# Kernel tuning notes

Measured on AMD Instinct MI355X. Metric: run time of the kernel, lower is better.

The kernel has to match this reference:

```python
import jax, jax.numpy as jnp
import numpy as np

B, S, H = 1, 2048, 2048
NH = 16
NOPE, ROPE, VD = 128, 64, 128
QD = NOPE + ROPE
QLR, KVLR = 1536, 512
INH, IND, ITOPK = 4, 32, 512
EPS = 1e-6
SCALE = QD ** -0.5
ISCALE = IND ** -0.5


def rms_norm(x, w, eps=EPS):
    x = x * jax.lax.rsqrt(jnp.mean(x * x, axis=-1, keepdims=True) + eps)
    return w * x


def rotate_half(x):
    h = x.shape[-1] // 2
    return jnp.concatenate([-x[..., h:], x[..., :h]], axis=-1)


def setup_inputs():
    key = jax.random.key(0)
    ks = jax.random.split(key, 9)
    # real RoPE tables, theta=10000
    inv = 1.0 / (10000.0 ** (np.arange(0, ROPE, 2, dtype=np.float64) / ROPE))
    freqs = np.outer(np.arange(S, dtype=np.float64), inv)
    emb = np.concatenate([freqs, freqs], axis=-1)
    return {
        "x": jax.random.normal(ks[0], (B, S, H), jnp.float32),
        "cos": jnp.asarray(np.cos(emb), jnp.float32),
        "sin": jnp.asarray(np.sin(emb), jnp.float32),
        "q_a_w": jax.random.normal(ks[1], (QLR, H), jnp.float32) * 0.02,
        "q_a_norm_w": jnp.ones((QLR,), jnp.float32),
        "q_b_w": jax.random.normal(ks[2], (NH * QD, QLR), jnp.float32) * 0.02,
        "kv_a_w": jax.random.normal(ks[3], (KVLR + ROPE, H), jnp.float32) * 0.02,
        "kv_a_norm_w": jnp.ones((KVLR,), jnp.float32),
        "kv_b_w": jax.random.normal(ks[4], (NH * (NOPE + VD), KVLR), jnp.float32) * 0.02,
        "o_w": jax.random.normal(ks[5], (H, NH * VD), jnp.float32) * 0.02,
        "idx_q_w": jax.random.normal(ks[6], (INH * IND, H), jnp.float32) * 0.02,
        "idx_k_w": jax.random.normal(ks[7], (INH * IND, H), jnp.float32) * 0.02,
    }


def mla_forward(x, cos, sin, q_a_w, q_a_norm_w, q_b_w, kv_a_w, kv_a_norm_w,
                kv_b_w, o_w, idx_q_w, idx_k_w):
    b, s, _ = x.shape
    # low-rank Q: q_b(norm(q_a(x)))
    q = rms_norm(x @ q_a_w.T, q_a_norm_w) @ q_b_w.T
    q = q.reshape(b, s, NH, QD).transpose(0, 2, 1, 3)          # [b,H,s,QD]
    q_nope, q_pe = q[..., :NOPE], q[..., NOPE:]
    # low-rank KV: kv_a -> (compressed_kv, k_pe)
    kv_a = x @ kv_a_w.T                                         # [b,s,KVLR+ROPE]
    compressed_kv, k_pe = kv_a[..., :KVLR], kv_a[..., KVLR:]
    k_pe = k_pe[:, None]                                        # [b,1,s,ROPE]
    kv = (rms_norm(compressed_kv, kv_a_norm_w) @ kv_b_w.T)
    kv = kv.reshape(b, s, NH, NOPE + VD).transpose(0, 2, 1, 3)  # [b,H,s,NOPE+VD]
    k_nope, v = kv[..., :NOPE], kv[..., NOPE:]
    # decoupled RoPE on the rope sub-dim only
    c, sn = cos[None, None], sin[None, None]                    # [1,1,s,ROPE]
    q_pe = q_pe * c + rotate_half(q_pe) * sn
    k_pe = k_pe * c + rotate_half(k_pe) * sn
    qf = jnp.concatenate([q_nope, q_pe], axis=-1)               # [b,H,s,QD]
    kf = jnp.concatenate(
        [k_nope, jnp.broadcast_to(k_pe, (b, NH, s, ROPE))], axis=-1)
    scores = jnp.einsum('bhqd,bhkd->bhqk', qf, kf) * SCALE
    # indexer: mean-over-heads scores -> top-k allowed key positions per query
    iq = (x @ idx_q_w.T).reshape(b, s, INH, IND).transpose(0, 2, 1, 3)
    ik = (x @ idx_k_w.T).reshape(b, s, INH, IND).transpose(0, 2, 1, 3)
    iscores = jnp.einsum('bhqd,bhkd->bhqk', iq, ik) * ISCALE
    iscores = iscores.mean(axis=1)                              # [b,s,s]
    _, topk_idx = jax.lax.top_k(iscores, ITOPK)                 # [b,s,topk]
    allowed = jnp.zeros((b, s, s), bool).at[
        jnp.arange(b)[:, None, None],
        jnp.arange(s)[None, :, None],
        topk_idx].set(True)
    causal = jnp.tril(jnp.ones((s, s), bool))
    mask = allowed[:, None] & causal[None, None]                # [b,1,s,s] & causal
    scores = jnp.where(mask, scores, jnp.float32(-1e9))
    attn = jax.nn.softmax(scores, axis=-1)
    out = jnp.einsum('bhqk,bhkd->bhqd', attn, v)
    out = out.transpose(0, 2, 1, 3).reshape(b, s, NH * VD)
    return out @ o_w.T


def reference(x, cos, sin, q_a_w, q_a_norm_w, q_b_w, kv_a_w, kv_a_norm_w,
              kv_b_w, o_w, idx_q_w, idx_k_w):
    return mla_forward(x, cos, sin, q_a_w, q_a_norm_w, q_b_w, kv_a_w,
                       kv_a_norm_w, kv_b_w, o_w, idx_q_w, idx_k_w)
```

## Files before the change

### kernel.cpp

```cpp
#include <hip/hip_runtime.h>
#include <hip/hip_bf16.h>
#include <stdint.h>

#define S_LEN  2048
#define NHEADS 16
#define D_NOPE 128
#define D_ROPE 64
#define D_V    128
#define D_Q    192
#define ITOPK  512

static constexpr float ATT_SCALE = 0.07216878364870322f;
static constexpr float ISC4      = 0.04419417382415922f;
static constexpr float RMS_EPS   = 1e-6f;

typedef __bf16 bf16x8 __attribute__((ext_vector_type(8)));
typedef float  f32x4  __attribute__((ext_vector_type(4)));

__device__ __forceinline__ float b2f(unsigned short u) {
    union { unsigned int i; float f; } x; x.i = ((unsigned int)u) << 16; return x.f;
}
__device__ __forceinline__ unsigned short f2b(float f) {
    union { float f; unsigned int i; } x; x.f = f;
    unsigned int lsb = (x.i >> 16) & 1;
    x.i += 0x7fffu + lsb;
    return (unsigned short)(x.i >> 16);
}

__device__ __forceinline__ void gload16(const unsigned short* g, unsigned short* l)
{
    __builtin_amdgcn_global_load_lds(
        (const __attribute__((address_space(1))) unsigned int*)g,
        (__attribute__((address_space(3))) unsigned int*)l, 16, 0, 0);
}

__global__ __launch_bounds__(256)
void cast_f32_bf16(const float* __restrict__ src, unsigned short* __restrict__ dst, int n4)
{
    int i = blockIdx.x * 256 + threadIdx.x;
    if (i < n4) {
        float4 v = ((const float4*)src)[i];
        ushort4 o;
        o.x = f2b(v.x); o.y = f2b(v.y); o.z = f2b(v.z); o.w = f2b(v.w);
        ((ushort4*)dst)[i] = o;
    }
}

__global__ __launch_bounds__(256)
void gemm_f32_nt(const float* __restrict__ A, int lda,
                 const float* __restrict__ B, int ldb,
                 float* __restrict__ C, int M, int N, float alpha, int kChunk)
{
    __shared__ float As[16][132];
    __shared__ float Bs[16][132];
    const int row0 = blockIdx.y * 128;
    const int col0 = blockIdx.x * 128;
    const int t  = threadIdx.x;
    const int tx = t & 15, ty = t >> 4;
    const int kStart = blockIdx.z * kChunk;
    C += (size_t)blockIdx.z * M * N;

    float acc[8][8] = {};

    for (int k0 = kStart; k0 < kStart + kChunk; k0 += 16) {
#pragma unroll
        for (int i = 0; i < 2; i++) {
            int f = t + i * 256;
            int r = f >> 2;
            int kq = (f & 3) << 2;
            int gr = row0 + r;
            float4 va = make_float4(0.f, 0.f, 0.f, 0.f);
            if (gr < M) va = *(const float4*)(A + (size_t)gr * lda + k0 + kq);
            As[kq + 0][r] = va.x; As[kq + 1][r] = va.y;
            As[kq + 2][r] = va.z; As[kq + 3][r] = va.w;
            int gc = col0 + r;
            float4 vb = make_float4(0.f, 0.f, 0.f, 0.f);
            if (gc < N) vb = *(const float4*)(B + (size_t)gc * ldb + k0 + kq);
            Bs[kq + 0][r] = vb.x; Bs[kq + 1][r] = vb.y;
            Bs[kq + 2][r] = vb.z; Bs[kq + 3][r] = vb.w;
        }
        __syncthreads();
#pragma unroll
        for (int kk = 0; kk < 16; kk++) {
            float4 A0 = *(const float4*)&As[kk][ty * 8];
            float4 A1 = *(const float4*)&As[kk][ty * 8 + 4];
            float4 B0 = *(const float4*)&Bs[kk][tx * 8];
            float4 B1 = *(const float4*)&Bs[kk][tx * 8 + 4];
            float a[8] = {A0.x, A0.y, A0.z, A0.w, A1.x, A1.y, A1.z, A1.w};
            float b[8] = {B0.x, B0.y, B0.z, B0.w, B1.x, B1.y, B1.z, B1.w};
#pragma unroll
            for (int i = 0; i < 8; i++)
#pragma unroll
                for (int j = 0; j < 8; j++)
                    acc[i][j] = fmaf(a[i], b[j], acc[i][j]);
        }
        __syncthreads();
    }

#pragma unroll
    for (int i = 0; i < 8; i++) {
        int r = row0 + ty * 8 + i;
        if (r >= M) continue;
#pragma unroll
        for (int j = 0; j < 8; j++) {
            int c = col0 + tx * 8 + j;
            if (c >= N) continue;
            C[(size_t)r * N + c] = acc[i][j] * alpha;
        }
    }
}

__global__ __launch_bounds__(256)
void reduceN_k(const float* __restrict__ p, float* __restrict__ out, int n4, int parts)
{
    int i = blockIdx.x * 256 + threadIdx.x;
    if (i < n4) {
        const float4* a = (const float4*)p;
        float4 o = a[i];
        for (int z = 1; z < parts; z++) {
            float4 r = a[i + (size_t)z * n4];
            o.x += r.x; o.y += r.y; o.z += r.z; o.w += r.w;
        }
        ((float4*)out)[i] = o;
    }
}

template<bool OUTBF16>
__global__ __launch_bounds__(256)
void gemm_bf16_nt(const unsigned short* __restrict__ A, int lda, int aStep,
                  const unsigned short* __restrict__ B, int ldb, int bStep,
                  void* __restrict__ Cv, int ldc, int cStep,
                  int M, int N, int K, float alpha)
{
    __shared__ unsigned short As[128 * 32];
    __shared__ unsigned short Bs[128 * 32];
    A += (size_t)blockIdx.z * aStep;
    B += (size_t)blockIdx.z * bStep;
    unsigned short* Cb = (unsigned short*)Cv + (size_t)blockIdx.z * cStep;
    float*          Cf = (float*)Cv          + (size_t)blockIdx.z * cStep;

    const int t = threadIdx.x;
    const int row0 = blockIdx.y * 128, col0 = blockIdx.x * 128;
    const int w = t >> 6, l = t & 63;
    const int wr = (w >> 1) * 64, wc = (w & 1) * 64;
    const int fr = l & 15, fk = l >> 4;

    f32x4 acc[4][4] = {};

    const int sr = t >> 2, ss = t & 3;

    for (int k0 = 0; k0 < K; k0 += 32) {
#pragma unroll
        for (int c = 0; c < 2; c++) {
            int r  = sr + c * 64;
            int ga = min(row0 + r, M - 1);
            int gb = min(col0 + r, N - 1);
            gload16(A + (size_t)ga * lda + k0 + ss * 8, As + (c * 256 + t) * 8);
            gload16(B + (size_t)gb * ldb + k0 + ss * 8, Bs + (c * 256 + t) * 8);
        }
        __syncthreads();

        bf16x8 af[4], bfr[4];
#pragma unroll
        for (int mi = 0; mi < 4; mi++) {
            int ra = wr + mi * 16 + fr;
            af[mi] = *(const bf16x8*)((const char*)As + ra * 64 + fk * 16);
        }
#pragma unroll
        for (int nj = 0; nj < 4; nj++) {
            int rb = wc + nj * 16 + fr;
            bfr[nj] = *(const bf16x8*)((const char*)Bs + rb * 64 + fk * 16);
        }
#pragma unroll
        for (int mi = 0; mi < 4; mi++)
#pragma unroll
            for (int nj = 0; nj < 4; nj++)
                acc[mi][nj] = __builtin_amdgcn_mfma_f32_16x16x32_bf16(
                                  af[mi], bfr[nj], acc[mi][nj], 0, 0, 0);
        __syncthreads();
    }

#pragma unroll
    for (int mi = 0; mi < 4; mi++)
#pragma unroll
        for (int nj = 0; nj < 4; nj++)
#pragma unroll
            for (int rg = 0; rg < 4; rg++) {
                int rr = row0 + wr + mi * 16 + fk * 4 + rg;
                int cc = col0 + wc + nj * 16 + fr;
                if (rr < M && cc < N) {
                    float v = acc[mi][nj][rg] * alpha;
                    if constexpr (OUTBF16) Cb[(size_t)rr * ldc + cc] = f2b(v);
                    else                   Cf[(size_t)rr * ldc + cc] = v;
                }
            }
}

__global__ __launch_bounds__(256)
void rms_bf16_inplace(unsigned short* x, const float* __restrict__ w, int n)
{
    __shared__ float red[256];
    const int row = blockIdx.x, t = threadIdx.x;
    unsigned short* ip = x + (size_t)row * n;
    float ss = 0.f;
    for (int i = t; i < n; i += 256) { float v = b2f(ip[i]); ss = fmaf(v, v, ss); }
    red[t] = ss; __syncthreads();
    for (int s2 = 128; s2; s2 >>= 1) { if (t < s2) red[t] += red[t + s2]; __syncthreads(); }
    float rs = rsqrtf(red[0] / (float)n + RMS_EPS);
    for (int i = t; i < n; i += 256) ip[i] = f2b(b2f(ip[i]) * rs * w[i]);
}

__global__ __launch_bounds__(256)
void rms_f32_bf16(const float* __restrict__ in, unsigned short* __restrict__ out,
                  const float* __restrict__ w, int n, int in_stride, int out_stride)
{
    __shared__ float red[256];
    const int row = blockIdx.x, t = threadIdx.x;
    const float* ip = in + (size_t)row * in_stride;
    float ss = 0.f;
    for (int i = t; i < n; i += 256) { float v = ip[i]; ss = fmaf(v, v, ss); }
    red[t] = ss; __syncthreads();
    for (int s2 = 128; s2; s2 >>= 1) { if (t < s2) red[t] += red[t + s2]; __syncthreads(); }
    float rs = rsqrtf(red[0] / (float)n + RMS_EPS);
    unsigned short* op = out + (size_t)row * out_stride;
    for (int i = t; i < n; i += 256) op[i] = f2b(ip[i] * rs * w[i]);
}

__global__ __launch_bounds__(256)
void rope_q_k(const unsigned short* __restrict__ qbuf, const float* __restrict__ cosb,
              const float* __restrict__ sinb, unsigned short* __restrict__ qec)
{
    int idx = blockIdx.x * 256 + threadIdx.x;
    int s = idx >> 9, h = (idx >> 5) & 15, d = idx & 31;
    const unsigned short* qp = qbuf + ((size_t)s * NHEADS + h) * D_Q + D_NOPE;
    float x1 = b2f(qp[d]), x2 = b2f(qp[d + 32]);
    const float* cr = cosb + (size_t)s * D_ROPE;
    const float* sr = sinb + (size_t)s * D_ROPE;
    unsigned short* op = qec + ((size_t)s * NHEADS + h) * 576 + 512;
    op[d]      = f2b(x1 * cr[d]      - x2 * sr[d]);
    op[d + 32] = f2b(x2 * cr[d + 32] + x1 * sr[d + 32]);
}

__global__ __launch_bounds__(256)
void rope_kpe_k(const float* __restrict__ kv_a, const float* __restrict__ cosb,
                const float* __restrict__ sinb, unsigned short* __restrict__ klat)
{
    int idx = blockIdx.x * 256 + threadIdx.x;
    int s = idx >> 5, d = idx & 31;
    const float* kp = kv_a + (size_t)s * 576 + 512;
    float x1 = kp[d], x2 = kp[d + 32];
    const float* cr = cosb + (size_t)s * D_ROPE;
    const float* sr = sinb + (size_t)s * D_ROPE;
    unsigned short* op = klat + (size_t)s * 576 + 512;
    op[d]      = f2b(x1 * cr[d]      - x2 * sr[d]);
    op[d + 32] = f2b(x2 * cr[d + 32] + x1 * sr[d + 32]);
}

__global__ __launch_bounds__(256)
void wkt_k(const unsigned short* __restrict__ kvbw, unsigned short* __restrict__ wkt)
{
    __shared__ unsigned short tile[32][520];
    const int h = blockIdx.x, dc = blockIdx.y, t = threadIdx.x;
    for (int i = t; i < 32 * 64; i += 256) {
        int d = i >> 6, c8 = (i & 63) * 8;
        uint4 v = *(const uint4*)(kvbw + ((size_t)(h * 256 + dc * 32 + d)) * 512 + c8);
        *(uint4*)&tile[d][c8] = v;
    }
    __syncthreads();
    for (int i = t; i < 512 * 4; i += 256) {
        int c = i >> 2, d8 = (i & 3) * 8;
        unsigned short tmp[8];
#pragma unroll
        for (int j = 0; j < 8; j++) tmp[j] = tile[d8 + j][c];
        *(uint4*)(wkt + ((size_t)h * 512 + c) * 128 + dc * 32 + d8) = *(uint4*)tmp;
    }
}

__global__ __launch_bounds__(256)
void ckvsum_k(const unsigned short* __restrict__ klat, float* __restrict__ part)
{
    const int b = blockIdx.x, t = threadIdx.x;
    float s0 = 0.f, s1 = 0.f;
    for (int r = 0; r < 128; r++) {
        const unsigned short* row = klat + (size_t)(b * 128 + r) * 576;
        s0 += b2f(row[t]); s1 += b2f(row[t + 256]);
    }
    part[b * 512 + t] = s0; part[b * 512 + t + 256] = s1;
}
__global__ __launch_bounds__(256)
void ckvmean_k(const float* __restrict__ part, float* __restrict__ mean)
{
    int t = blockIdx.x * 256 + threadIdx.x;
    if (t < 512) {
        float s = 0.f;
        for (int b = 0; b < 16; b++) s += part[b * 512 + t];
        mean[t] = s * (1.f / 2048.f);
    }
}

__global__ __launch_bounds__(256)
void topk_mask_k(const float* __restrict__ iscores, uint32_t* __restrict__ mask)
{
    const int q = blockIdx.x, t = threadIdx.x;
    const int w = t >> 6, l = t & 63;
    __shared__ uint32_t u[S_LEN];
    __shared__ int hist4[4][256];
    __shared__ int sfx[257];
    __shared__ int wtot[4];
    __shared__ uint32_t mw[64];
    __shared__ int sh_b, sh_R;

    for (int i = t; i < S_LEN; i += 256) {
        uint32_t b = __float_as_uint(iscores[(size_t)q * S_LEN + i]);
        u[i] = (b & 0x80000000u) ? ~b : (b | 0x80000000u);
    }
    if (t < 64) mw[t] = 0u;

    uint32_t prefix = 0;
    int R = ITOPK;
#pragma unroll 1
    for (int shift = 24; shift >= 0; shift -= 8) {
        hist4[0][t] = 0; hist4[1][t] = 0; hist4[2][t] = 0; hist4[3][t] = 0;
        __syncthreads();
        uint32_t pmask = (shift == 24) ? 0u : (0xFFFFFFFFu << (shift + 8));
        for (int i = t; i < S_LEN; i += 256) {
            uint32_t v = u[i];
            if ((v & pmask) == prefix)
                atomicAdd(&hist4[w][(v >> shift) & 255], 1);
        }
        __syncthreads();
        int x = hist4[0][255 - t] + hist4[1][255 - t] + hist4[2][255 - t] + hist4[3][255 - t];
#pragma unroll
        for (int d = 1; d < 64; d <<= 1) {
            int y = __shfl_up(x, d);
            if (l >= d) x += y;
        }
        if (l == 63) wtot[w] = x;
        __syncthreads();
        for (int ww = 0; ww < w; ww++) x += wtot[ww];
        sfx[255 - t] = x;
        if (t == 0) sfx[256] = 0;
        __syncthreads();
        if (sfx[t] >= R && sfx[t + 1] < R) { sh_b = t; sh_R = R - sfx[t + 1]; }
        __syncthreads();
        prefix |= (uint32_t)sh_b << shift;
        R = sh_R;
        __syncthreads();
    }
    const uint32_t T = prefix;
    const int need = R;

    for (int i = t; i < S_LEN; i += 256) {
        uint32_t v = u[i];
        bool sel = v > T;
        if (!sel && v == T) {
            int rank = 0;
            for (int j = 0; j < i; j++) rank += (u[j] == T) ? 1 : 0;
            sel = rank < need;
        }
        if (sel) atomicOr(&mw[i >> 5], 1u << (i & 31));
    }
    __syncthreads();
    if (t < 64) mask[(size_t)q * 64 + t] = mw[t];
}

__global__ __launch_bounds__(256, 4)
void attn_lat_k(const unsigned short* __restrict__ qec,
                const unsigned short* __restrict__ klat,
                const uint32_t* __restrict__ mask,
                const float* __restrict__ ckvmean,
                unsigned short* __restrict__ ov)
{
    const int qi = blockIdx.x, t = threadIdx.x;
    const int w = t >> 6, l = t & 63;
    const int c16 = l & 15, g = l >> 4;

    __shared__ unsigned short kl[512];
    __shared__ uint32_t wds[64];
    __shared__ int pfx[65];
    __shared__ float wred[4][16];
    __shared__ float linv[16];
    __shared__ unsigned short PB[16][520];
    __shared__ unsigned short CT[256][40];

    kl[t] = 0; kl[t + 256] = 0;
    if (t < 64) {
        uint32_t wd = mask[(size_t)qi * 64 + t];
        int rem = qi - t * 32;
        if (rem < 0) wd = 0u;
        else if (rem < 31) wd &= ((2u << rem) - 1u);
        wds[t] = wd;
        pfx[t] = __popc(wd);
    }
    __syncthreads();
    if (t == 0) {
        int s = 0;
        for (int i = 0; i < 64; i++) { int cc = pfx[i]; pfx[i] = s; s += cc; }
        pfx[64] = s;
    }
    __syncthreads();
    const int nv = pfx[64];

    if (nv == 0) {
        for (int i = t; i < 16 * 512; i += 256) {
            int h = i >> 9, c = i & 511;
            ov[((size_t)qi * 16 + h) * 512 + c] = f2b(ckvmean[c]);
        }
        return;
    }

    if (t < 64) {
        int pos = pfx[t];
        uint32_t wd = wds[t];
        while (wd) { int b = __ffs(wd) - 1; wd &= wd - 1; kl[pos++] = (unsigned short)(t * 32 + b); }
    }
    __syncthreads();

    const int ntile = (nv + 63) >> 6;

    f32x4 acc[8] = {};
    uint32_t kb[8];
#pragma unroll
    for (int tt = 0; tt < 8; tt++)
        kb[tt] = (uint32_t)kl[tt * 64 + w * 16 + c16] * 1152u;

    const unsigned short* qrow = qec + (size_t)qi * (16 * 576);
#pragma unroll 2
    for (int ks = 0; ks < 18; ks++) {
        bf16x8 af = *(const bf16x8*)(qrow + c16 * 576 + ks * 32 + g * 8);
#pragma unroll
        for (int tt = 0; tt < 8; tt++) {
            if (tt < ntile) {
                bf16x8 bf = *(const bf16x8*)((const char*)klat + (kb[tt] + (uint32_t)(ks * 64 + g * 16)));
                acc[tt] = __builtin_amdgcn_mfma_f32_16x16x32_bf16(af, bf, acc[tt], 0, 0, 0);
            }
        }
    }

    float m4[4];
#pragma unroll
    for (int r = 0; r < 4; r++) {
        float mm = -1e30f;
#pragma unroll
        for (int tt = 0; tt < 8; tt++) {
            if (tt < ntile) {
                int kp = tt * 64 + w * 16 + c16;
                float s = (kp < nv) ? acc[tt][r] * ATT_SCALE : -1e30f;
                acc[tt][r] = s;
                mm = fmaxf(mm, s);
            }
        }
#pragma unroll
        for (int o = 8; o; o >>= 1) mm = fmaxf(mm, __shfl_xor(mm, o));
        m4[r] = mm;
    }
    if (c16 == 0) {
#pragma unroll
        for (int r = 0; r < 4; r++) wred[w][g * 4 + r] = m4[r];
    }
    __syncthreads();
#pragma unroll
    for (int r = 0; r < 4; r++) {
        int h = g * 4 + r;
        m4[r] = fmaxf(fmaxf(wred[0][h], wred[1][h]), fmaxf(wred[2][h], wred[3][h]));
    }
    __syncthreads();

    float s4[4] = {0.f, 0.f, 0.f, 0.f};
#pragma unroll
    for (int tt = 0; tt < 8; tt++) {
        if (tt < ntile) {
            int kp = tt * 64 + w * 16 + c16;
#pragma unroll
            for (int r = 0; r < 4; r++) {
                float e = __expf(acc[tt][r] - m4[r]);
                s4[r] += e;
                PB[g * 4 + r][kp] = f2b(e);
            }
        }
    }
#pragma unroll
    for (int r = 0; r < 4; r++) {
        float ss = s4[r];
#pragma unroll
        for (int o = 8; o; o >>= 1) ss += __shfl_xor(ss, o);
        s4[r] = ss;
    }
    if (c16 == 0) {
#pragma unroll
        for (int r = 0; r < 4; r++) wred[w][g * 4 + r] = s4[r];
    }
    __syncthreads();
    if (t < 16) linv[t] = 1.f / (wred[0][t] + wred[1][t] + wred[2][t] + wred[3][t]);

    f32x4 pv[8] = {};
    const int nkc = (nv + 31) >> 5;
    const int k2 = t >> 4, lg = t & 15;
    const int cp = (k2 ^ ((lg & 3) << 2)) * 2;
    uint4 stg[4];

#define LOADKEYS(HT, KC) do { \
        uint32_t kb0 = (uint32_t)kl[(KC) * 32 + 2 * k2] * 1152u; \
        uint32_t kb1 = (uint32_t)kl[(KC) * 32 + 2 * k2 + 1] * 1152u; \
        const uint4* s0 = (const uint4*)((const char*)klat + kb0 + (HT) * 512 + lg * 32); \
        const uint4* s1 = (const uint4*)((const char*)klat + kb1 + (HT) * 512 + lg * 32); \
        stg[0] = s0[0]; stg[1] = s0[1]; stg[2] = s1[0]; stg[3] = s1[1]; \
    } while (0)

    LOADKEYS(0, 0);
#pragma unroll
    for (int ht = 0; ht < 2; ht++) {
        for (int kc = 0; kc < nkc; kc++) {
            __syncthreads();
            {
#pragma unroll
                for (int v4 = 0; v4 < 2; v4++) {
                    uint4 a4 = stg[v4], b4 = stg[v4 + 2];
                    int la = lg * 16 + v4 * 8;
                    *(uint32_t*)&CT[la + 0][cp] = (a4.x & 0xFFFFu) | (b4.x << 16);
                    *(uint32_t*)&CT[la + 1][cp] = (a4.x >> 16) | (b4.x & 0xFFFF0000u);
                    *(uint32_t*)&CT[la + 2][cp] = (a4.y & 0xFFFFu) | (b4.y << 16);
                    *(uint32_t*)&CT[la + 3][cp] = (a4.y >> 16) | (b4.y & 0xFFFF0000u);
                    *(uint32_t*)&CT[la + 4][cp] = (a4.z & 0xFFFFu) | (b4.z << 16);
                    *(uint32_t*)&CT[la + 5][cp] = (a4.z >> 16) | (b4.z & 0xFFFF0000u);
                    *(uint32_t*)&CT[la + 6][cp] = (a4.w & 0xFFFFu) | (b4.w << 16);
                    *(uint32_t*)&CT[la + 7][cp] = (a4.w >> 16) | (b4.w & 0xFFFF0000u);
                }
            }
            if (kc + 1 < nkc) LOADKEYS(ht, kc + 1);
            else if (ht == 0) LOADKEYS(1, 0);
            __syncthreads();
            bf16x8 pa = *(const bf16x8*)(&PB[c16][kc * 32 + g * 8]);
            __builtin_amdgcn_s_setprio(1);
#pragma unroll
            for (int nt = 0; nt < 4; nt++) {
                int rowh = w * 64 + nt * 16 + c16;
                bf16x8 cb = *(const bf16x8*)(&CT[rowh][(g ^ nt) * 8]);
                pv[ht * 4 + nt] = __builtin_amdgcn_mfma_f32_16x16x32_bf16(
                                      pa, cb, pv[ht * 4 + nt], 0, 0, 0);
            }
            __builtin_amdgcn_s_setprio(0);
        }
    }
#undef LOADKEYS

#pragma unroll
    for (int ht = 0; ht < 2; ht++)
#pragma unroll
        for (int nt = 0; nt < 4; nt++)
#pragma unroll
            for (int r = 0; r < 4; r++) {
                int h = g * 4 + r;
                int lat = ht * 256 + w * 64 + nt * 16 + c16;
                ov[((size_t)qi * 16 + h) * 512 + lat] = f2b(pv[ht * 4 + nt][r] * linv[h]);
            }
}

extern "C" void kernel_launch(void* const* d_in, const int* in_sizes, int n_in,
                              void* d_out, int out_size, void* d_ws, size_t ws_size,
                              hipStream_t stream)
{
    const float* x       = (const float*)d_in[0];
    const float* cosb    = (const float*)d_in[1];
    const float* sinb    = (const float*)d_in[2];
    const float* q_a_w   = (const float*)d_in[3];
    const float* q_a_nw  = (const float*)d_in[4];
    const float* q_b_w   = (const float*)d_in[5];
    const float* kv_a_w  = (const float*)d_in[6];
    const float* kv_a_nw = (const float*)d_in[7];
    const float* kv_b_w  = (const float*)d_in[8];
    const float* o_w     = (const float*)d_in[9];
    const float* idx_q_w = (const float*)d_in[10];
    const float* idx_k_w = (const float*)d_in[11];
    (void)in_sizes; (void)n_in; (void)out_size; (void)ws_size;

    typedef unsigned short u16;
    char* ws = (char*)d_ws;
    u16*      xb   = (u16*)(ws + 0);
    u16*      qaw  = (u16*)(ws + 8388608);
    u16*      kvaw = (u16*)(ws + 14680064);
    u16*      qbw  = (u16*)(ws + 17039360);
    u16*      q_a  = (u16*)(ws + 26476544);
    float*    kv_a = (float*)(ws + 32768000);
    u16*      qec  = (u16*)(ws + 0);
    u16*      wkt  = (u16*)(ws + 37748736);
    float*    iw   = (float*)(ws + 39845888);
    float*    ipc  = (float*)(ws + 41943040);
    float*    iqik = (float*)(ws + 58720256);
    float*    isc  = (float*)(ws + 60817408);
    u16*      ov   = (u16*)(ws + 37748736);
    u16*      qbuf = (u16*)(ws + 71303168);
    u16*      aoutb= (u16*)(ws + 71303168);
    u16*      klat = (u16*)(ws + 83886080);
    u16*      kvbw = (u16*)(ws + 86245376);
    u16*      owb  = (u16*)(ws + 90439680);
    uint32_t* mask = (uint32_t*)(ws + 98828288);
    float*    ckvm = (float*)(ws + 99352576);
    float*    cprt = (float*)(ws + 99354624);

    dim3 blk(256);
    auto cast = [&](const float* s, u16* d, int n) {
        cast_f32_bf16<<<dim3((n / 4 + 255) / 256), blk, 0, stream>>>(s, d, n / 4);
    };

    cast(x, xb, 2048 * 2048);
    cast(q_a_w, qaw, 1536 * 2048);
    cast(kv_a_w, kvaw, 576 * 2048);
    cast(q_b_w, qbw, 3072 * 1536);
    cast(kv_b_w, kvbw, 4096 * 512);
    cast(o_w, owb, 2048 * 2048);

    gemm_bf16_nt<true ><<<dim3(12, 16), blk, 0, stream>>>(xb, 2048, 0, qaw, 2048, 0,
                                                          q_a, 1536, 0, 2048, 1536, 2048, 1.f);
    gemm_bf16_nt<false><<<dim3(5, 16),  blk, 0, stream>>>(xb, 2048, 0, kvaw, 2048, 0,
                                                          kv_a, 576, 0, 2048, 576, 2048, 1.f);
    rms_bf16_inplace<<<2048, blk, 0, stream>>>(q_a, q_a_nw, 1536);
    rms_f32_bf16<<<2048, blk, 0, stream>>>(kv_a, klat, kv_a_nw, 512, 576, 576);
    rope_kpe_k<<<256, blk, 0, stream>>>(kv_a, cosb, sinb, klat);

    gemm_bf16_nt<true ><<<dim3(24, 16), blk, 0, stream>>>(q_a, 1536, 0, qbw, 1536, 0,
                                                          qbuf, 3072, 0, 2048, 3072, 1536, 1.f);
    wkt_k<<<dim3(16, 4), blk, 0, stream>>>(kvbw, wkt);

    gemm_bf16_nt<true ><<<dim3(4, 16, 16), blk, 0, stream>>>(qbuf, 3072, 192, wkt, 128, 512 * 128,
                                                             qec, 9216, 576, 2048, 512, 128, 1.f);
    rope_q_k<<<4096, blk, 0, stream>>>(qbuf, cosb, sinb, qec);

    ckvsum_k<<<16, blk, 0, stream>>>(klat, cprt);
    ckvmean_k<<<2, blk, 0, stream>>>(cprt, ckvm);

    hipMemcpyAsync(iw,                 idx_q_w, 128 * 2048 * 4, hipMemcpyDeviceToDevice, stream);
    hipMemcpyAsync(iw + 128 * 2048,    idx_k_w, 128 * 2048 * 4, hipMemcpyDeviceToDevice, stream);
    gemm_f32_nt<<<dim3(2, 16, 8), blk, 0, stream>>>(x, 2048, iw, 2048, ipc, 2048, 256, 1.f, 256);
    reduceN_k<<<512, blk, 0, stream>>>(ipc, iqik, 131072, 8);
    gemm_f32_nt<<<dim3(16, 16, 1), blk, 0, stream>>>(iqik, 256, iqik + 128, 256,
                                                     isc, 2048, 2048, ISC4, 128);
    topk_mask_k<<<2048, blk, 0, stream>>>(isc, mask);

    attn_lat_k<<<2048, blk, 0, stream>>>(qec, klat, mask, ckvm, ov);

    gemm_bf16_nt<true ><<<dim3(1, 16, 16), blk, 0, stream>>>(ov, 8192, 512,
                                                             kvbw + 128 * 512, 512, 256 * 512,
                                                             aoutb, 2048, 128, 2048, 128, 512, 1.f);
    gemm_bf16_nt<false><<<dim3(16, 16), blk, 0, stream>>>(aoutb, 2048, 0, owb, 2048, 0,
                                                          (float*)d_out, 2048, 0, 2048, 2048, 2048, 1.f);
}
```

Before: 615.8 us.

## Merge q_a/kv_a projections into one GEMM and fuse casts and KV norm+RoPE

The six separate f32-to-bf16 cast launches become a single cast kernel that routes by index. That kernel writes the q_a and kv_a weights into one concatenated buffer, so a single GEMM with N=2112 replaces the two down-projection GEMMs; the old kv_a GEMM launched only 80 blocks. The KV RMS norm and k_pe RoPE are fused into one kernel that reads the bf16 GEMM output. The workspace layout is reshuffled to reuse freed regions. This removes launch overhead and an underfilled GEMM, but kv_a is now stored as bf16 rather than f32 before the norm and RoPE, which slightly lowers precision.

```diff
diff --git a/kernel.cpp b/kernel.cpp
--- a/kernel.cpp
+++ b/kernel.cpp
@@ -35,15 +35,27 @@
 }
 
 __global__ __launch_bounds__(256)
-void cast_f32_bf16(const float* __restrict__ src, unsigned short* __restrict__ dst, int n4)
+void cast_all(const float* __restrict__ x,    const float* __restrict__ qaw_,
+              const float* __restrict__ kvaw_, const float* __restrict__ qbw_,
+              const float* __restrict__ kvbw_, const float* __restrict__ ow_,
+              unsigned short* __restrict__ xb,   unsigned short* __restrict__ wcat,
+              unsigned short* __restrict__ qbw,  unsigned short* __restrict__ kvbw,
+              unsigned short* __restrict__ owb)
 {
     int i = blockIdx.x * 256 + threadIdx.x;
-    if (i < n4) {
-        float4 v = ((const float4*)src)[i];
-        ushort4 o;
-        o.x = f2b(v.x); o.y = f2b(v.y); o.z = f2b(v.z); o.w = f2b(v.w);
-        ((ushort4*)dst)[i] = o;
-    }
+    const float* s; unsigned short* d; int off;
+    if      (i < 1048576) { s = x;     d = xb;              off = 0;       }
+    else if (i < 1835008) { s = qaw_;  d = wcat;            off = 1048576; }
+    else if (i < 2129920) { s = kvaw_; d = wcat + 3145728;  off = 1835008; }
+    else if (i < 3309568) { s = qbw_;  d = qbw;             off = 2129920; }
+    else if (i < 3833856) { s = kvbw_; d = kvbw;            off = 3309568; }
+    else if (i < 4882432) { s = ow_;   d = owb;             off = 3833856; }
+    else return;
+    int j = i - off;
+    float4 v = ((const float4*)s)[j];
+    ushort4 o;
+    o.x = f2b(v.x); o.y = f2b(v.y); o.z = f2b(v.z); o.w = f2b(v.w);
+    ((ushort4*)d)[j] = o;
 }
 
 __global__ __launch_bounds__(256)
@@ -197,11 +209,11 @@
 }
 
 __global__ __launch_bounds__(256)
-void rms_bf16_inplace(unsigned short* x, const float* __restrict__ w, int n)
+void rms_bf16_inplace(unsigned short* x, const float* __restrict__ w, int n, int stride)
 {
     __shared__ float red[256];
     const int row = blockIdx.x, t = threadIdx.x;
-    unsigned short* ip = x + (size_t)row * n;
+    unsigned short* ip = x + (size_t)row * stride;
     float ss = 0.f;
     for (int i = t; i < n; i += 256) { float v = b2f(ip[i]); ss = fmaf(v, v, ss); }
     red[t] = ss; __syncthreads();
@@ -211,19 +223,28 @@
 }
 
 __global__ __launch_bounds__(256)
-void rms_f32_bf16(const float* __restrict__ in, unsigned short* __restrict__ out,
-                  const float* __restrict__ w, int n, int in_stride, int out_stride)
+void rmsrope_klat(const unsigned short* __restrict__ xa, const float* __restrict__ w,
+                  const float* __restrict__ cosb, const float* __restrict__ sinb,
+                  unsigned short* __restrict__ klat)
 {
     __shared__ float red[256];
     const int row = blockIdx.x, t = threadIdx.x;
-    const float* ip = in + (size_t)row * in_stride;
-    float ss = 0.f;
-    for (int i = t; i < n; i += 256) { float v = ip[i]; ss = fmaf(v, v, ss); }
-    red[t] = ss; __syncthreads();
+    const unsigned short* ip = xa + (size_t)row * 2112 + 1536;
+    float v0 = b2f(ip[t]), v1 = b2f(ip[t + 256]);
+    red[t] = v0 * v0 + v1 * v1; __syncthreads();
     for (int s2 = 128; s2; s2 >>= 1) { if (t < s2) red[t] += red[t + s2]; __syncthreads(); }
-    float rs = rsqrtf(red[0] / (float)n + RMS_EPS);
-    unsigned short* op = out + (size_t)row * out_stride;
-    for (int i = t; i < n; i += 256) op[i] = f2b(ip[i] * rs * w[i]);
+    float rs = rsqrtf(red[0] / 512.f + RMS_EPS);
+    unsigned short* op = klat + (size_t)row * 576;
+    op[t]       = f2b(v0 * rs * w[t]);
+    op[t + 256] = f2b(v1 * rs * w[t + 256]);
+    if (t < 32) {
+        int d = t;
+        float x1 = b2f(ip[512 + d]), x2 = b2f(ip[512 + d + 32]);
+        const float* cr = cosb + (size_t)row * D_ROPE;
+        const float* sr = sinb + (size_t)row * D_ROPE;
+        op[512 + d]      = f2b(x1 * cr[d]      - x2 * sr[d]);
+        op[512 + d + 32] = f2b(x2 * cr[d + 32] + x1 * sr[d + 32]);
+    }
 }
 
 __global__ __launch_bounds__(256)
@@ -237,21 +258,6 @@
     const float* cr = cosb + (size_t)s * D_ROPE;
     const float* sr = sinb + (size_t)s * D_ROPE;
     unsigned short* op = qec + ((size_t)s * NHEADS + h) * 576 + 512;
-    op[d]      = f2b(x1 * cr[d]      - x2 * sr[d]);
-    op[d + 32] = f2b(x2 * cr[d + 32] + x1 * sr[d + 32]);
-}
-
-__global__ __launch_bounds__(256)
-void rope_kpe_k(const float* __restrict__ kv_a, const float* __restrict__ cosb,
-                const float* __restrict__ sinb, unsigned short* __restrict__ klat)
-{
-    int idx = blockIdx.x * 256 + threadIdx.x;
-    int s = idx >> 5, d = idx & 31;
-    const float* kp = kv_a + (size_t)s * 576 + 512;
-    float x1 = kp[d], x2 = kp[d + 32];
-    const float* cr = cosb + (size_t)s * D_ROPE;
-    const float* sr = sinb + (size_t)s * D_ROPE;
-    unsigned short* op = klat + (size_t)s * 576 + 512;
     op[d]      = f2b(x1 * cr[d]      - x2 * sr[d]);
     op[d + 32] = f2b(x2 * cr[d + 32] + x1 * sr[d + 32]);
 }
@@ -577,19 +583,17 @@
     typedef unsigned short u16;
     char* ws = (char*)d_ws;
     u16*      xb   = (u16*)(ws + 0);
-    u16*      qaw  = (u16*)(ws + 8388608);
-    u16*      kvaw = (u16*)(ws + 14680064);
+    u16*      wcat = (u16*)(ws + 8388608);
     u16*      qbw  = (u16*)(ws + 17039360);
-    u16*      q_a  = (u16*)(ws + 26476544);
-    float*    kv_a = (float*)(ws + 32768000);
+    u16*      xa   = (u16*)(ws + 26476544);
     u16*      qec  = (u16*)(ws + 0);
     u16*      wkt  = (u16*)(ws + 37748736);
-    float*    iw   = (float*)(ws + 39845888);
-    float*    ipc  = (float*)(ws + 41943040);
-    float*    iqik = (float*)(ws + 58720256);
-    float*    isc  = (float*)(ws + 60817408);
+    float*    ipc  = (float*)(ws + 37748736);
+    float*    iqik = (float*)(ws + 37748736);
+    float*    isc  = (float*)(ws + 39845888);
     u16*      ov   = (u16*)(ws + 37748736);
     u16*      qbuf = (u16*)(ws + 71303168);
+    float*    iw   = (float*)(ws + 71303168);
     u16*      aoutb= (u16*)(ws + 71303168);
     u16*      klat = (u16*)(ws + 83886080);
     u16*      kvbw = (u16*)(ws + 86245376);
@@ -599,26 +603,16 @@
     float*    cprt = (float*)(ws + 99354624);
 
     dim3 blk(256);
-    auto cast = [&](const float* s, u16* d, int n) {
-        cast_f32_bf16<<<dim3((n / 4 + 255) / 256), blk, 0, stream>>>(s, d, n / 4);
-    };
-
-    cast(x, xb, 2048 * 2048);
-    cast(q_a_w, qaw, 1536 * 2048);
-    cast(kv_a_w, kvaw, 576 * 2048);
-    cast(q_b_w, qbw, 3072 * 1536);
-    cast(kv_b_w, kvbw, 4096 * 512);
-    cast(o_w, owb, 2048 * 2048);
-
-    gemm_bf16_nt<true ><<<dim3(12, 16), blk, 0, stream>>>(xb, 2048, 0, qaw, 2048, 0,
-                                                          q_a, 1536, 0, 2048, 1536, 2048, 1.f);
-    gemm_bf16_nt<false><<<dim3(5, 16),  blk, 0, stream>>>(xb, 2048, 0, kvaw, 2048, 0,
-                                                          kv_a, 576, 0, 2048, 576, 2048, 1.f);
-    rms_bf16_inplace<<<2048, blk, 0, stream>>>(q_a, q_a_nw, 1536);
-    rms_f32_bf16<<<2048, blk, 0, stream>>>(kv_a, klat, kv_a_nw, 512, 576, 576);
-    rope_kpe_k<<<256, blk, 0, stream>>>(kv_a, cosb, sinb, klat);
-
-    gemm_bf16_nt<true ><<<dim3(24, 16), blk, 0, stream>>>(q_a, 1536, 0, qbw, 1536, 0,
+
+    cast_all<<<19072, blk, 0, stream>>>(x, q_a_w, kv_a_w, q_b_w, kv_b_w, o_w,
+                                        xb, wcat, qbw, kvbw, owb);
+
+    gemm_bf16_nt<true ><<<dim3(17, 16), blk, 0, stream>>>(xb, 2048, 0, wcat, 2048, 0,
+                                                          xa, 2112, 0, 2048, 2112, 2048, 1.f);
+    rms_bf16_inplace<<<2048, blk, 0, stream>>>(xa, q_a_nw, 1536, 2112);
+    rmsrope_klat<<<2048, blk, 0, stream>>>(xa, kv_a_nw, cosb, sinb, klat);
+
+    gemm_bf16_nt<true ><<<dim3(24, 16), blk, 0, stream>>>(xa, 2112, 0, qbw, 1536, 0,
                                                           qbuf, 3072, 0, 2048, 3072, 1536, 1.f);
     wkt_k<<<dim3(16, 4), blk, 0, stream>>>(kvbw, wkt);
 
@@ -629,8 +623,8 @@
     ckvsum_k<<<16, blk, 0, stream>>>(klat, cprt);
     ckvmean_k<<<2, blk, 0, stream>>>(cprt, ckvm);
 
-    hipMemcpyAsync(iw,                 idx_q_w, 128 * 2048 * 4, hipMemcpyDeviceToDevice, stream);
-    hipMemcpyAsync(iw + 128 * 2048,    idx_k_w, 128 * 2048 * 4, hipMemcpyDeviceToDevice, stream);
+    hipMemcpyAsync(iw,              idx_q_w, 128 * 2048 * 4, hipMemcpyDeviceToDevice, stream);
+    hipMemcpyAsync(iw + 128 * 2048, idx_k_w, 128 * 2048 * 4, hipMemcpyDeviceToDevice, stream);
     gemm_f32_nt<<<dim3(2, 16, 8), blk, 0, stream>>>(x, 2048, iw, 2048, ipc, 2048, 256, 1.f, 256);
     reduceN_k<<<512, blk, 0, stream>>>(ipc, iqik, 131072, 8);
     gemm_f32_nt<<<dim3(16, 16, 1), blk, 0, stream>>>(iqik, 256, iqik + 128, 256,
```

New measurement: 568.7 us. 1.08x faster.
